# Kernel optimization log

Hardware: AMD Instinct MI355X
Metric: run time of the kernel (lower is better)

## Reference

```python
import jax, jax.numpy as jnp
import numpy as np

N_QUBITS = 20
EVO_SUPPORT = (2, 5)
CHAIN_QUBIT = 0


def _apply_operator(state, op, support):
    """Apply batched operator op (2^k, 2^k, B) to state (2,)*n + (B,) on `support` qubits.

    Faithful to pyqtorch's apply_operator: reshape op to (2,)*2k + (B,) and contract
    the support axes, keeping the batch axis aligned.
    """
    n = state.ndim - 1
    k = len(support)
    B = state.shape[-1]
    op = op.reshape((2,) * (2 * k) + (B,))
    letters = 'abcdefghijklmnopqrstuvwxyz'
    s_l = list(letters[:n])          # state qubit axes
    b = letters[n]                   # batch axis
    out_l = list(letters[n + 1:n + 1 + k])
    in_l = [s_l[q] for q in support]
    op_str = ''.join(out_l) + ''.join(in_l) + b
    st_str = ''.join(s_l) + b
    res = list(s_l)
    for q, o in zip(support, out_l):
        res[q] = o
    return jnp.einsum(f"{op_str},{st_str}->{''.join(res) + b}", op, state)


def setup_inputs() -> dict:
    key = jax.random.key(0)
    ks = jax.random.split(key, 6)
    B = 16
    dim = 2 ** N_QUBITS
    return {
        'state_re': jax.random.normal(ks[0], (dim, B), jnp.float32),
        'state_im': jax.random.normal(ks[1], (dim, B), jnp.float32),
        'hmat_re': jax.random.normal(ks[2], (4, 4, B), jnp.float32),
        'hmat_im': jax.random.normal(ks[3], (4, 4, B), jnp.float32),
        'theta': jax.random.uniform(ks[4], (8, B), jnp.float32),
        'tvals': jax.random.uniform(ks[5], (B,), jnp.float32),
    }


def reference(state_re, state_im, hmat_re, hmat_im, theta, tvals):
    n = N_QUBITS
    B = state_re.shape[-1]
    state = (state_re + 1j * state_im).astype(jnp.complex64).reshape((2,) * n + (B,))

    # --- PyQComposedBlock: chain of single-qubit RX gates composed via reduce(bmm, reversed) ---
    half = 0.5 * theta                      # (N_ops, B)
    c = jnp.cos(half).astype(jnp.complex64)
    s = jnp.sin(half).astype(jnp.complex64)
    # U_k: [[c, -i s], [-i s, c]] per op, batch-first layout (N_ops, B, 2, 2)
    U = jnp.stack([jnp.stack([c, -1j * s], axis=-1),
                   jnp.stack([-1j * s, c], axis=-1)], axis=-2)
    acc = U[-1]
    for i in range(U.shape[0] - 2, -1, -1):  # reduce(bmm, reversed(ops)): U_{N-1} @ ... @ U_0
        acc = acc @ U[i]
    state = _apply_operator(state, jnp.moveaxis(acc, 0, -1), (CHAIN_QUBIT,))

    # --- PyQHamiltonianEvolution: U = exp(-i t H) on a 2-qubit support ---
    A = (hmat_re + 1j * hmat_im).astype(jnp.complex64)       # (4, 4, B)
    H = 0.5 * (A + jnp.conj(jnp.swapaxes(A, 0, 1)))          # Hermitian generator
    Hb = jnp.moveaxis(H, -1, 0)                              # (B, 4, 4)
    evals, V = jnp.linalg.eigh(Hb)                           # H Hermitian -> exact matrix exp
    phase = jnp.exp(-1j * tvals[:, None] * evals)            # (B, 4)
    Ue = jnp.einsum('bij,bj,bkj->bik', V, phase.astype(jnp.complex64), jnp.conj(V))
    state = _apply_operator(state, jnp.moveaxis(Ue, 0, -1), EVO_SUPPORT)

    # --- Observable: total magnetization sum_q Z_q (AddPyQOperation of diagonal Z ops) ---
    w = jnp.zeros((2,) * n, jnp.float32)
    z = jnp.array([1.0, -1.0], jnp.float32)
    for q in range(n):
        w = w + z.reshape((1,) * q + (2,) + (1,) * (n - 1 - q))
    opsi = state * w[..., None]
    # expectation Re<psi|O|psi> per batch element
    return jnp.real(jnp.sum(jnp.conj(state) * opsi, axis=tuple(range(n))))
```

## Files before the change

kernel.cpp:

```cpp
#include <hip/hip_runtime.h>
#include <math.h>

constexpr int NQ     = 20;
constexpr int DIM    = 1 << NQ;
constexpr int B      = 16;
constexpr int GROUPS = 1 << 17;
constexpr int GPB    = 32;
constexpr int NBLK   = GROUPS / GPB;
constexpr int NTHR   = 512;


__global__ __launch_bounds__(256) void prep_kernel(
    const float* __restrict__ hre, const float* __restrict__ him,
    const float* __restrict__ theta, const float* __restrict__ tv,
    float* __restrict__ ws, float* __restrict__ out) {
  __shared__ double Mre[16][16], Mim[16][16];
  __shared__ double Are[16][16], Aim[16][16];
  __shared__ double Bre[16][16], Bim[16][16];
  __shared__ double nrm[16][4];
  __shared__ int    scl[16];
  __shared__ int    scmax_s;

  int t = threadIdx.x;
  int b = t >> 4, e = t & 15, i = e >> 2, j = e & 3;

  if (t < 16) out[t] = 0.f;
  if (t == 0) scmax_s = 0;

  if (e == 0) {
    double th = 0.0;
    for (int k = 0; k < 8; k++) th += (double)theta[k * B + b];
    th *= 0.5;
    ws[b]     = (float)cos(th);
    ws[B + b] = (float)sin(th);
  }

  {
    double tt  = (double)tv[b];
    double are = hre[(i*4+j)*B + b], aim = him[(i*4+j)*B + b];
    double cre = hre[(j*4+i)*B + b], cim = him[(j*4+i)*B + b];
    double Hre = 0.5*(are + cre), Him = 0.5*(aim - cim);
    Mre[b][e] = tt * Him;
    Mim[b][e] = -tt * Hre;
  }
  __syncthreads();

  if (j == 0) {
    double r = 0.0;
    for (int m = 0; m < 4; m++) r += fabs(Mre[b][i*4+m]) + fabs(Mim[b][i*4+m]);
    nrm[b][i] = r;
  }
  __syncthreads();
  if (e == 0) {
    double ninf = fmax(fmax(nrm[b][0], nrm[b][1]), fmax(nrm[b][2], nrm[b][3]));
    int sc = 0;
    while (ninf > 0.25 && sc < 40) { ninf *= 0.5; sc++; }
    scl[b] = sc;
    atomicMax(&scmax_s, sc);
  }
  __syncthreads();
  int sc = scl[b];
  int scmax = scmax_s;
  {
    double scale = ldexp(1.0, -sc);
    Mre[b][e] *= scale; Mim[b][e] *= scale;
  }
  Are[b][e] = (i == j) ? 1.0 : 0.0;
  Aim[b][e] = 0.0;
  __syncthreads();

  double (*Tr)[16] = Are; double (*Ti)[16] = Aim;
  double (*Pr)[16] = Bre; double (*Pi)[16] = Bim;

  for (int k = 13; k >= 1; k--) {
    double rr = 0.0, ii = 0.0;
    for (int m = 0; m < 4; m++) {
      double mr = Mre[b][i*4+m], mi = Mim[b][i*4+m];
      double xr = Tr[b][m*4+j],  xi = Ti[b][m*4+j];
      rr += mr*xr - mi*xi;
      ii += mr*xi + mi*xr;
    }
    double inv = 1.0 / (double)k;
    Pr[b][e] = rr*inv + ((i == j) ? 1.0 : 0.0);
    Pi[b][e] = ii*inv;
    { double (*s)[16] = Tr; Tr = Pr; Pr = s; s = Ti; Ti = Pi; Pi = s; }
    __syncthreads();
  }
  for (int q = 0; q < scmax; q++) {
    double rr, ii;
    if (q < sc) {
      rr = 0.0; ii = 0.0;
      for (int m = 0; m < 4; m++) {
        double xr = Tr[b][i*4+m], xi = Ti[b][i*4+m];
        double yr = Tr[b][m*4+j], yi = Ti[b][m*4+j];
        rr += xr*yr - xi*yi;
        ii += xr*yi + xi*yr;
      }
    } else { rr = Tr[b][e]; ii = Ti[b][e]; }
    Pr[b][e] = rr; Pi[b][e] = ii;
    { double (*s)[16] = Tr; Tr = Pr; Pr = s; s = Ti; Ti = Pi; Pi = s; }
    __syncthreads();
  }

  float* ue = ws + 2*B + b*32;
  ue[e*2]     = (float)Tr[b][e];
  ue[e*2 + 1] = (float)Ti[b][e];
}

__global__ __launch_bounds__(NTHR) void fused_kernel(
    const float* __restrict__ sre, const float* __restrict__ sim,
    const float* __restrict__ ws, float* __restrict__ out) {
  __shared__ float st[16 * 512];
  __shared__ float red[16];

  int t = threadIdx.x;
  int g0 = blockIdx.x * GPB;
  int base0 = (g0 & 0x3FFF) | ((g0 & 0xC000) << 1) | ((g0 & 0x10000) << 2);

  #pragma unroll
  for (int p = 0; p < 4; p++) {
    int ci    = p * 512 + t;
    int panel = ci >> 7;
    int w     = (ci & 127) << 2;
    int j     = panel >> 1;
    const float* src = (panel & 1) ? sim : sre;
    int off = ((((j >> 2) & 1) << 19) | (((j >> 1) & 1) << 17) | ((j & 1) << 14));
    float4 v = *(const float4*)(src + (base0 + off) * 16 + w);
    *(float4*)&st[panel * 512 + w] = v;
  }
  if (t < 16) red[t] = 0.f;

  int b  = t & 15;
  int gl = t >> 4;
  float c = ws[b], s = ws[B + b];
  float ur[4][4], ui[4][4];
  {
    const float* ue = ws + 2 * B + b * 32;
    #pragma unroll
    for (int i = 0; i < 4; i++) {
      float4 p0 = *(const float4*)(ue + i * 8);
      float4 p1 = *(const float4*)(ue + i * 8 + 4);
      ur[i][0] = p0.x; ui[i][0] = p0.y; ur[i][1] = p0.z; ui[i][1] = p0.w;
      ur[i][2] = p1.x; ui[i][2] = p1.y; ur[i][3] = p1.z; ui[i][3] = p1.w;
    }
  }
  __syncthreads();

  float ar[8], ai[8];
  #pragma unroll
  for (int j = 0; j < 8; j++) {
    ar[j] = st[(2 * j) * 512 + t];
    ai[j] = st[(2 * j + 1) * 512 + t];
  }

  #pragma unroll
  for (int j = 0; j < 4; j++) {
    float xr = ar[j], xi = ai[j], yr = ar[j+4], yi = ai[j+4];
    ar[j]   = c*xr + s*yi;   ai[j]   = c*xi - s*yr;
    ar[j+4] = s*xi + c*yr;   ai[j+4] = c*yi - s*xr;
  }

  int base = base0 + gl;
  int pc = __popc(base);
  float wb = (float)(17 - 2*pc);
  float acc = 0.f;
  #pragma unroll
  for (int h = 0; h < 2; h++) {
    float w0 = wb + (h ? -1.f : 1.f);
    #pragma unroll
    for (int k = 0; k < 4; k++) {
      float rr = 0.f, ii = 0.f;
      #pragma unroll
      for (int m = 0; m < 4; m++) {
        float xr = ar[h*4+m], xi = ai[h*4+m];
        rr = fmaf(ur[k][m], xr, rr); rr = fmaf(-ui[k][m], xi, rr);
        ii = fmaf(ur[k][m], xi, ii); ii = fmaf(ui[k][m], xr, ii);
      }
      int sb = ((k>>1)&1) + (k&1);
      float w = w0 + (float)(2 - 2*sb);
      acc = fmaf(rr*rr + ii*ii, w, acc);
    }
  }

  acc += __shfl_xor(acc, 16, 64);
  acc += __shfl_xor(acc, 32, 64);

  if ((t & 63) < 16) atomicAdd(&red[t & 15], acc);
  __syncthreads();
  if (t < 16) atomicAdd(&out[t], red[t]);
}

extern "C" void kernel_launch(void* const* d_in, const int* in_sizes, int n_in,
                              void* d_out, int out_size, void* d_ws, size_t ws_size,
                              hipStream_t stream) {
  const float* sre = (const float*)d_in[0];
  const float* sim = (const float*)d_in[1];
  const float* hre = (const float*)d_in[2];
  const float* him = (const float*)d_in[3];
  const float* th  = (const float*)d_in[4];
  const float* tv  = (const float*)d_in[5];

  float* ws = (float*)d_ws;
  float* out = (float*)d_out;

  prep_kernel<<<1, 256, 0, stream>>>(hre, him, th, tv, ws, out);
  fused_kernel<<<NBLK, NTHR, 0, stream>>>(sre, sim, ws, out);
}
```

Before: 184.9 us.

## Use persistent blocks with direct global-to-LDS loads and a two-stage reduction

Result: faster. 177.7 us (-3.9%).

```diff
diff --git a/kernel.cpp b/kernel.cpp
--- a/kernel.cpp
+++ b/kernel.cpp
@@ -6,14 +6,16 @@
 constexpr int B      = 16;
 constexpr int GROUPS = 1 << 17;
 constexpr int GPB    = 32;
-constexpr int NBLK   = GROUPS / GPB;
+constexpr int TILES  = GROUPS / GPB;
+constexpr int NBLK   = 1024;
+constexpr int TPB    = TILES / NBLK;
 constexpr int NTHR   = 512;
 
 
 __global__ __launch_bounds__(256) void prep_kernel(
     const float* __restrict__ hre, const float* __restrict__ him,
     const float* __restrict__ theta, const float* __restrict__ tv,
-    float* __restrict__ ws, float* __restrict__ out) {
+    float* __restrict__ ws) {
   __shared__ double Mre[16][16], Mim[16][16];
   __shared__ double Are[16][16], Aim[16][16];
   __shared__ double Bre[16][16], Bim[16][16];
@@ -24,7 +26,6 @@
   int t = threadIdx.x;
   int b = t >> 4, e = t & 15, i = e >> 2, j = e & 3;
 
-  if (t < 16) out[t] = 0.f;
   if (t == 0) scmax_s = 0;
 
   if (e == 0) {
@@ -107,27 +108,13 @@
   ue[e*2 + 1] = (float)Ti[b][e];
 }
 
-__global__ __launch_bounds__(NTHR) void fused_kernel(
+__global__ __launch_bounds__(NTHR, 6) void fused_kernel(
     const float* __restrict__ sre, const float* __restrict__ sim,
-    const float* __restrict__ ws, float* __restrict__ out) {
+    const float* __restrict__ ws, float* __restrict__ partial) {
   __shared__ float st[16 * 512];
   __shared__ float red[16];
 
   int t = threadIdx.x;
-  int g0 = blockIdx.x * GPB;
-  int base0 = (g0 & 0x3FFF) | ((g0 & 0xC000) << 1) | ((g0 & 0x10000) << 2);
-
-  #pragma unroll
-  for (int p = 0; p < 4; p++) {
-    int ci    = p * 512 + t;
-    int panel = ci >> 7;
-    int w     = (ci & 127) << 2;
-    int j     = panel >> 1;
-    const float* src = (panel & 1) ? sim : sre;
-    int off = ((((j >> 2) & 1) << 19) | (((j >> 1) & 1) << 17) | ((j & 1) << 14));
-    float4 v = *(const float4*)(src + (base0 + off) * 16 + w);
-    *(float4*)&st[panel * 512 + w] = v;
-  }
   if (t < 16) red[t] = 0.f;
 
   int b  = t & 15;
@@ -144,42 +131,67 @@
       ur[i][2] = p1.x; ui[i][2] = p1.y; ur[i][3] = p1.z; ui[i][3] = p1.w;
     }
   }
-  __syncthreads();
-
-  float ar[8], ai[8];
-  #pragma unroll
-  for (int j = 0; j < 8; j++) {
-    ar[j] = st[(2 * j) * 512 + t];
-    ai[j] = st[(2 * j + 1) * 512 + t];
-  }
-
-  #pragma unroll
-  for (int j = 0; j < 4; j++) {
-    float xr = ar[j], xi = ai[j], yr = ar[j+4], yi = ai[j+4];
-    ar[j]   = c*xr + s*yi;   ai[j]   = c*xi - s*yr;
-    ar[j+4] = s*xi + c*yr;   ai[j+4] = c*yi - s*xr;
-  }
-
-  int base = base0 + gl;
-  int pc = __popc(base);
-  float wb = (float)(17 - 2*pc);
+
+  int l  = t & 63;
+  int wv = t >> 6;
   float acc = 0.f;
-  #pragma unroll
-  for (int h = 0; h < 2; h++) {
-    float w0 = wb + (h ? -1.f : 1.f);
-    #pragma unroll
-    for (int k = 0; k < 4; k++) {
-      float rr = 0.f, ii = 0.f;
+
+  for (int tt = 0; tt < TPB; tt++) {
+    int g0 = (blockIdx.x * TPB + tt) * GPB;
+    int base0 = (g0 & 0x3FFF) | ((g0 & 0xC000) << 1) | ((g0 & 0x10000) << 2);
+
+    #pragma unroll
+    for (int p = 0; p < 4; p++) {
+      int cb    = p * 512 + wv * 64;
+      int panel = cb >> 7;
+      int wofs  = (cb & 127) << 2;
+      int j     = panel >> 1;
+      const float* src = (panel & 1) ? sim : sre;
+      int off = (((j >> 2) & 1) << 19) | (((j >> 1) & 1) << 17) | ((j & 1) << 14);
+      const float* gsrc = src + (size_t)(base0 + off) * 16 + wofs + l * 4;
+      float* ldst = &st[panel * 512 + wofs];
+      __builtin_amdgcn_global_load_lds(
+          (const __attribute__((address_space(1))) void*)gsrc,
+          (__attribute__((address_space(3))) void*)ldst,
+          16, 0, 0);
+    }
+    __syncthreads();
+
+    float ar[8], ai[8];
+    #pragma unroll
+    for (int j = 0; j < 8; j++) {
+      ar[j] = st[(2 * j) * 512 + t];
+      ai[j] = st[(2 * j + 1) * 512 + t];
+    }
+
+    #pragma unroll
+    for (int j = 0; j < 4; j++) {
+      float xr = ar[j], xi = ai[j], yr = ar[j+4], yi = ai[j+4];
+      ar[j]   = c*xr + s*yi;   ai[j]   = c*xi - s*yr;
+      ar[j+4] = s*xi + c*yr;   ai[j+4] = c*yi - s*xr;
+    }
+
+    int base = base0 + gl;
+    int pc = __popc(base);
+    float wb = (float)(17 - 2*pc);
+    #pragma unroll
+    for (int h = 0; h < 2; h++) {
+      float w0 = wb + (h ? -1.f : 1.f);
       #pragma unroll
-      for (int m = 0; m < 4; m++) {
-        float xr = ar[h*4+m], xi = ai[h*4+m];
-        rr = fmaf(ur[k][m], xr, rr); rr = fmaf(-ui[k][m], xi, rr);
-        ii = fmaf(ur[k][m], xi, ii); ii = fmaf(ui[k][m], xr, ii);
+      for (int k = 0; k < 4; k++) {
+        float rr = 0.f, ii = 0.f;
+        #pragma unroll
+        for (int m = 0; m < 4; m++) {
+          float xr = ar[h*4+m], xi = ai[h*4+m];
+          rr = fmaf(ur[k][m], xr, rr); rr = fmaf(-ui[k][m], xi, rr);
+          ii = fmaf(ur[k][m], xi, ii); ii = fmaf(ui[k][m], xr, ii);
+        }
+        int sb = ((k>>1)&1) + (k&1);
+        float w = w0 + (float)(2 - 2*sb);
+        acc = fmaf(rr*rr + ii*ii, w, acc);
       }
-      int sb = ((k>>1)&1) + (k&1);
-      float w = w0 + (float)(2 - 2*sb);
-      acc = fmaf(rr*rr + ii*ii, w, acc);
-    }
+    }
+    __syncthreads();
   }
 
   acc += __shfl_xor(acc, 16, 64);
@@ -187,7 +199,23 @@
 
   if ((t & 63) < 16) atomicAdd(&red[t & 15], acc);
   __syncthreads();
-  if (t < 16) atomicAdd(&out[t], red[t]);
+  if (t < 16) partial[blockIdx.x * 16 + t] = red[t];
+}
+
+__global__ void reduce_kernel(const float* __restrict__ partial, float* __restrict__ out) {
+  int t = threadIdx.x;
+  int b = t & 15;
+  float acc = 0.f;
+  for (int i = t >> 4; i < NBLK; i += 16)
+    acc += partial[i * 16 + b];
+  acc += __shfl_xor(acc, 16, 64);
+  acc += __shfl_xor(acc, 32, 64);
+  __shared__ float red[16];
+  if (t < 16) red[t] = 0.f;
+  __syncthreads();
+  if ((t & 63) < 16) atomicAdd(&red[t & 15], acc);
+  __syncthreads();
+  if (t < 16) out[t] = red[t];
 }
 
 extern "C" void kernel_launch(void* const* d_in, const int* in_sizes, int n_in,
@@ -201,8 +229,9 @@
   const float* tv  = (const float*)d_in[5];
 
   float* ws = (float*)d_ws;
-  float* out = (float*)d_out;
-
-  prep_kernel<<<1, 256, 0, stream>>>(hre, him, th, tv, ws, out);
-  fused_kernel<<<NBLK, NTHR, 0, stream>>>(sre, sim, ws, out);
-}
+  float* partial = ws + 544;
+
+  prep_kernel<<<1, 256, 0, stream>>>(hre, him, th, tv, ws);
+  fused_kernel<<<NBLK, NTHR, 0, stream>>>(sre, sim, ws, partial);
+  reduce_kernel<<<1, 256, 0, stream>>>(partial, (float*)d_out);
+}
```
